# Kernel tuning notes

Hardware: AMD Instinct MI355X
Metric: run time of the kernel (lower is better)

The kernel has to match this reference:

```python
import jax, jax.numpy as jnp
import numpy as np

TRAIN_WAY = 5
TRAIN_SHOT = 5
N_LOCAL = 100  # == h*w, so Conv1d(kernel=stride=n_local) pools each class segment


def setup_inputs() -> dict:
    key = jax.random.key(0)
    k1, k2, k3 = jax.random.split(key, 3)
    t, wq, ws, c, h, w = 4, 75, 25, 640, 10, 10
    return {
        "query_feat": jax.random.normal(k1, (t, wq, c, h, w), dtype=jnp.float32),
        "support_feat": jax.random.normal(k2, (t, ws, c, h, w), dtype=jnp.float32),
        "conv_w": jax.random.normal(k3, (1, 1, N_LOCAL), dtype=jnp.float32) * 0.1,
        "conv_b": jnp.zeros((1,), dtype=jnp.float32),
    }


def reference(query_feat, support_feat, conv_w, conv_b):
    t, wq, c, h, w = query_feat.shape
    hw = h * w
    way, shot = TRAIN_WAY, TRAIN_SHOT

    # ---- support covariance per (t, way) ----
    s = support_feat.reshape(t, way * shot, c, hw).transpose(0, 1, 3, 2)  # (t, ws, hw, c)
    s = s.reshape(t, way, shot * hw, c)
    s = s - jnp.mean(s, axis=2, keepdims=True)
    cov = jnp.einsum('twnc,twnd->twcd', s, s) / (hw - 1)  # (t, way, c, c)

    # ---- query features centered over spatial positions ----
    q = query_feat.reshape(t, wq, c, hw).transpose(0, 1, 3, 2)  # (t, wq, hw, c)
    q = q - jnp.mean(q, axis=2, keepdims=True)

    # diag(Q @ Cov @ Q^T) == sum((Q @ Cov) * Q, -1)  -- same math, no hw x hw intermediate
    qc = jnp.einsum('tqnc,twcd->tqwnd', q, cov)          # (t, wq, way, hw, c)
    cov_sim = jnp.sum(qc * q[:, :, None], axis=-1)       # (t, wq, way, hw)

    # ---- LeakyReLU(0.2) -> Dropout (eval: identity) -> Conv1d(k=stride=hw) ----
    x = jnp.where(cov_sim >= 0, cov_sim, 0.2 * cov_sim)
    # conv with kernel=stride=hw over length way*hw == per-segment dot product
    score = jnp.einsum('tqwn,n->tqw', x, conv_w[0, 0]) + conv_b[0]
    return score  # (t, wq, way)
```

## Files before the change

kernel.cpp:

```cpp
#include <hip/hip_runtime.h>

#define T     4
#define WQ    75
#define C     640
#define HW    100
#define WAY   5
#define SHOT  5
#define NT    5
#define NPAIR 15

#define QOCT  14
#define QTS   (QOCT*128*8)
#define SOCT  64
#define STS   (SOCT*128*8)

#define WS_COVB_OFF  0
#define WS_QTB_OFF   9830400
#define WS_QTBW_OFF  52838400
#define WS_STB_OFF   95846400

typedef __attribute__((ext_vector_type(8)))  short bfrag8;
typedef __attribute__((ext_vector_type(16))) float f32x16;

__device__ __forceinline__ unsigned short f2bf(float x) {
    unsigned int u = __float_as_uint(x);
    return (unsigned short)((u + 0x7fffu + ((u >> 16) & 1u)) >> 16);
}
__device__ __forceinline__ float bflo(unsigned u) { return __uint_as_float(u << 16); }
__device__ __forceinline__ float bfhi(unsigned u) { return __uint_as_float(u & 0xffff0000u); }

__device__ __forceinline__ void pair_ij(int p, int& ti, int& tj) {
    int base = 0;
    #pragma unroll
    for (int a = 0; a < NT; ++a) {
        int cnt = NT - a;
        if (p < base + cnt) { ti = a; tj = a + (p - base); return; }
        base += cnt;
    }
    ti = 0; tj = 0;
}

#define LD2S 505
#define SROWS 8
#define NSPACK (20 * (C / SROWS))
struct SpackSh { float ld2[SROWS * LD2S]; float mpart2[SROWS][32]; float mean2[SROWS]; };
struct QpackSh { float ld[32 * 101]; float wl[HW]; float mpart[32][4]; float mean[32]; };
union PackSh { SpackSh s; QpackSh q; };

__global__ __launch_bounds__(256, 8)
void pack_kernel(const float* __restrict__ qf, const float* __restrict__ sf,
                 const float* __restrict__ convw, const float* __restrict__ bias,
                 unsigned short* __restrict__ stb, unsigned short* __restrict__ qtb,
                 unsigned short* __restrict__ qtbw, float* __restrict__ out) {
    __shared__ PackSh sh;
    int bid = blockIdx.x, tid = threadIdx.x;

    if (bid < NSPACK) {
        int rb = bid % 80, tw = bid / 80;
        int r0 = rb * SROWS;
        for (int sh_i = 0; sh_i < SHOT; ++sh_i) {
            const float* src = sf + ((size_t)(tw * SHOT + sh_i) * C + r0) * HW;
            if (tid < 200) {
                float4 v = ((const float4*)src)[tid];
                int f = tid * 4;
                int row = f / HW, n = f % HW;
                float* d = &sh.s.ld2[row * LD2S + sh_i * HW + n];
                d[0] = v.x; d[1] = v.y; d[2] = v.z; d[3] = v.w;
            }
        }
        __syncthreads();
        {
            int row = tid & 7, part = tid >> 3;
            float ps = 0.f;
            #pragma unroll
            for (int i = 0; i < 16; ++i) {
                int k = part * 16 + i;
                if (k < 500) ps += sh.s.ld2[row * LD2S + k];
            }
            sh.s.mpart2[row][part] = ps;
        }
        __syncthreads();
        if (tid < SROWS) {
            float s2 = 0.f;
            #pragma unroll
            for (int p2 = 0; p2 < 32; ++p2) s2 += sh.s.mpart2[tid][p2];
            sh.s.mean2[tid] = s2 * (1.0f / (SHOT * HW));
        }
        __syncthreads();
        #pragma unroll
        for (int it = 0; it < 2; ++it) {
            int task = tid + it * 256;
            int row = task & 7, oct = task >> 3;
            float m = sh.s.mean2[row];
            unsigned short ob[8] __attribute__((aligned(16)));
            #pragma unroll
            for (int j = 0; j < 8; ++j) {
                int k = oct * 8 + j;
                ob[j] = (k < 500) ? f2bf(sh.s.ld2[row * LD2S + k] - m) : (unsigned short)0;
            }
            int crow = r0 + row;
            int tile = crow >> 7, trow = crow & 127;
            size_t dst = ((((size_t)tw * NT + tile) * SOCT + oct) * 128 + trow) * 8;
            *(uint4*)(stb + dst) = *(uint4*)ob;
        }
    } else {
        int idx0 = bid - NSPACK;
        int cb = idx0 % 20, tq = idx0 / 20;
        if (idx0 == 0) {
            float b = bias[0];
            for (int i = tid; i < T * WQ * WAY; i += 256) out[i] = b;
        }
        if (tid < HW) sh.q.wl[tid] = convw[tid];
        const float* src = qf + ((size_t)tq * C + cb * 32) * HW;
        #pragma unroll
        for (int it = 0; it < 4; ++it) {
            int idx = tid + it * 256;
            if (idx < 800) {
                float4 v = ((const float4*)src)[idx];
                int f = idx * 4;
                int row = f / HW, n = f % HW;
                float* d = &sh.q.ld[row * 101 + n];
                d[0] = v.x; d[1] = v.y; d[2] = v.z; d[3] = v.w;
            }
        }
        __syncthreads();
        if (tid < 128) {
            int row = tid & 31, part = tid >> 5;
            float ps = 0.f;
            #pragma unroll
            for (int i = 0; i < 25; ++i) ps += sh.q.ld[row * 101 + part * 25 + i];
            sh.q.mpart[row][part] = ps;
        }
        __syncthreads();
        if (tid < 32) sh.q.mean[tid] = (sh.q.mpart[tid][0] + sh.q.mpart[tid][1]
                                      + sh.q.mpart[tid][2] + sh.q.mpart[tid][3]) * (1.0f / HW);
        __syncthreads();
        int crow0 = cb * 32;
        int tile = crow0 >> 7, trowbase = crow0 & 127;
        #pragma unroll
        for (int it = 0; it < 2; ++it) {
            int task = tid + it * 256;
            if (task < 32 * QOCT) {
                int row = task & 31, oct = task >> 5;
                float m = sh.q.mean[row];
                unsigned short ob[8] __attribute__((aligned(16)));
                unsigned short ow[8] __attribute__((aligned(16)));
                #pragma unroll
                for (int j = 0; j < 8; ++j) {
                    int n = oct * 8 + j;
                    float v = (n < HW) ? (sh.q.ld[row * 101 + n] - m) : 0.f;
                    float w = (n < HW) ? sh.q.wl[n] : 0.f;
                    ob[j] = f2bf(v); ow[j] = f2bf(v * w);
                }
                size_t dst = ((((size_t)tq * NT + tile) * QOCT + oct) * 128 + trowbase + row) * 8;
                *(uint4*)(qtb + dst)  = *(uint4*)ob;
                *(uint4*)(qtbw + dst) = *(uint4*)ow;
            }
        }
    }
}

__global__ __launch_bounds__(256, 3)
void cov_kernel(const unsigned short* __restrict__ stb, unsigned short* __restrict__ covb) {
    int bid = blockIdx.x, tid = threadIdx.x;
    int p = bid % NPAIR, tw = bid / NPAIR;
    int ti, tj; pair_ij(p, ti, tj);
    int lane = tid & 63, wave = tid >> 6;
    int qm = wave & 1, qn = wave >> 1, lh = lane >> 5, ls = lane & 31;
    int rA = qm * 64 + ls, rB = qn * 64 + ls;
    const unsigned short* Ab = stb + ((size_t)tw * NT + ti) * STS;
    const unsigned short* Bb = stb + ((size_t)tw * NT + tj) * STS;

    f32x16 acc[4];
    #pragma unroll
    for (int b = 0; b < 4; ++b)
        #pragma unroll
        for (int e = 0; e < 16; ++e) acc[b][e] = 0.f;

    #pragma unroll 4
    for (int s = 0; s < 32; ++s) {
        int oc = s * 2 + lh;
        const unsigned short* ap = Ab + (size_t)oc * 1024;
        const unsigned short* bp = Bb + (size_t)oc * 1024;
        bfrag8 a0 = *(const bfrag8*)&ap[rA * 8];
        bfrag8 a1 = *(const bfrag8*)&ap[(rA + 32) * 8];
        bfrag8 b0 = *(const bfrag8*)&bp[rB * 8];
        bfrag8 b1 = *(const bfrag8*)&bp[(rB + 32) * 8];
        acc[0] = __builtin_amdgcn_mfma_f32_32x32x16_bf16(a0, b0, acc[0], 0, 0, 0);
        acc[1] = __builtin_amdgcn_mfma_f32_32x32x16_bf16(a0, b1, acc[1], 0, 0, 0);
        acc[2] = __builtin_amdgcn_mfma_f32_32x32x16_bf16(a1, b0, acc[2], 0, 0, 0);
        acc[3] = __builtin_amdgcn_mfma_f32_32x32x16_bf16(a1, b1, acc[3], 0, 0, 0);
    }

    const float inv = 1.0f / (HW - 1);
    unsigned short* cbp = covb + ((size_t)tw * NPAIR + p) * 16384;
    #pragma unroll
    for (int b = 0; b < 4; ++b) {
        unsigned ow[8];
        #pragma unroll
        for (int wd = 0; wd < 8; ++wd)
            ow[wd] = (unsigned)f2bf(acc[b][2 * wd] * inv)
                   | ((unsigned)f2bf(acc[b][2 * wd + 1] * inv) << 16);
        size_t off = (size_t)((wave * 4 + b) * 64 + lane) * 16;
        *(uint4*)(cbp + off)     = *(uint4*)&ow[0];
        *(uint4*)(cbp + off + 8) = *(uint4*)&ow[4];
    }
}

#define CSTEP (NPAIR * 16384)
#define LOADW(dst, src) { \
    _Pragma("unroll") \
    for (int b = 0; b < 4; ++b) { \
        dst[2*b]   = *(const uint4*)((src) + b * 1024); \
        dst[2*b+1] = *(const uint4*)((src) + b * 1024 + 8); } }
#define FROB(buf, sout) { \
    float s0 = 0.f, s1 = 0.f, s2 = 0.f, s3 = 0.f; \
    _Pragma("unroll") \
    for (int b = 0; b < 4; ++b) { \
        _Pragma("unroll") \
        for (int h = 0; h < 2; ++h) { \
            uint4 u = buf[2*b + h]; \
            int e = h * 8; \
            s0 += bflo(u.x) * acc[b][e + 0] + bfhi(u.x) * acc[b][e + 1]; \
            s1 += bflo(u.y) * acc[b][e + 2] + bfhi(u.y) * acc[b][e + 3]; \
            s2 += bflo(u.z) * acc[b][e + 4] + bfhi(u.z) * acc[b][e + 5]; \
            s3 += bflo(u.w) * acc[b][e + 6] + bfhi(u.w) * acc[b][e + 7]; } } \
    sout = (s0 + s1) + (s2 + s3); }

__global__ __launch_bounds__(256, 2)
void score_kernel(const unsigned short* __restrict__ qtb, const unsigned short* __restrict__ qtbw,
                  const unsigned short* __restrict__ covb, float* __restrict__ out) {
    __shared__ float red[4][WAY];
    int orig = blockIdx.x;
    int xcd = orig & 7, slot = orig >> 3;
    int wgid = (xcd < 4) ? (xcd * 563 + slot) : (2252 + (xcd - 4) * 562 + slot);
    int p = wgid % NPAIR;
    int tq = wgid / NPAIR;
    int t = tq / WQ, q = tq % WQ;
    int ti, tj; pair_ij(p, ti, tj);
    int tid = threadIdx.x, lane = tid & 63, wave = tid >> 6;
    int qm = wave & 1, qn = wave >> 1, lh = lane >> 5, ls = lane & 31;
    int rA = qm * 64 + ls, rB = qn * 64 + ls;
    float mult = (ti == tj) ? 1.0f : 2.0f;

    const unsigned short* Ab = qtbw + ((size_t)(t * WQ + q) * NT + ti) * QTS;
    const unsigned short* Bb = qtb  + ((size_t)(t * WQ + q) * NT + tj) * QTS;
    const unsigned short* cb0 = covb + ((size_t)(t * WAY) * NPAIR + p) * 16384
                              + (size_t)(wave * 4096 + lane * 16);

    uint4 cuA[8], cuB[8];
    LOADW(cuA, cb0)

    f32x16 acc[4];
    #pragma unroll
    for (int b = 0; b < 4; ++b)
        #pragma unroll
        for (int e = 0; e < 16; ++e) acc[b][e] = 0.f;

    #pragma unroll
    for (int s = 0; s < 7; ++s) {
        int oc = s * 2 + lh;
        const unsigned short* ap = Ab + (size_t)oc * 1024;
        const unsigned short* bp = Bb + (size_t)oc * 1024;
        bfrag8 a0 = *(const bfrag8*)&ap[rA * 8];
        bfrag8 a1 = *(const bfrag8*)&ap[(rA + 32) * 8];
        bfrag8 b0 = *(const bfrag8*)&bp[rB * 8];
        bfrag8 b1 = *(const bfrag8*)&bp[(rB + 32) * 8];
        acc[0] = __builtin_amdgcn_mfma_f32_32x32x16_bf16(a0, b0, acc[0], 0, 0, 0);
        acc[1] = __builtin_amdgcn_mfma_f32_32x32x16_bf16(a0, b1, acc[1], 0, 0, 0);
        acc[2] = __builtin_amdgcn_mfma_f32_32x32x16_bf16(a1, b0, acc[2], 0, 0, 0);
        acc[3] = __builtin_amdgcn_mfma_f32_32x32x16_bf16(a1, b1, acc[3], 0, 0, 0);
    }

    float sw[WAY];
    LOADW(cuB, cb0 + 1 * CSTEP)
    FROB(cuA, sw[0])
    LOADW(cuA, cb0 + 2 * CSTEP)
    FROB(cuB, sw[1])
    LOADW(cuB, cb0 + 3 * CSTEP)
    FROB(cuA, sw[2])
    LOADW(cuA, cb0 + 4 * CSTEP)
    FROB(cuB, sw[3])
    FROB(cuA, sw[4])

    #pragma unroll
    for (int w = 0; w < WAY; ++w) {
        float v = sw[w] * mult;
        #pragma unroll
        for (int off2 = 32; off2 > 0; off2 >>= 1) v += __shfl_down(v, off2);
        if (lane == 0) red[wave][w] = v;
    }
    __syncthreads();
    if (tid < WAY) {
        float tot = red[0][tid] + red[1][tid] + red[2][tid] + red[3][tid];
        atomicAdd(&out[(size_t)(t * WQ + q) * WAY + tid], tot);
    }
}

extern "C" void kernel_launch(void* const* d_in, const int* in_sizes, int n_in,
                              void* d_out, int out_size, void* d_ws, size_t ws_size,
                              hipStream_t stream) {
    const float* qf = (const float*)d_in[0];
    const float* sf = (const float*)d_in[1];
    const float* cw = (const float*)d_in[2];
    const float* cb = (const float*)d_in[3];
    float* out = (float*)d_out;

    unsigned short* covb = (unsigned short*)((char*)d_ws + WS_COVB_OFF);
    unsigned short* qtb  = (unsigned short*)((char*)d_ws + WS_QTB_OFF);
    unsigned short* qtbw = (unsigned short*)((char*)d_ws + WS_QTBW_OFF);
    unsigned short* stb  = (unsigned short*)((char*)d_ws + WS_STB_OFF);

    pack_kernel<<<NSPACK + 6000, 256, 0, stream>>>(qf, sf, cw, cb, stb, qtb, qtbw, out);
    cov_kernel<<<300, 256, 0, stream>>>(stb, covb);
    score_kernel<<<4500, 256, 0, stream>>>(qtb, qtbw, covb, out);
}
```

Baseline: 220.5 us.

## Process two queries per score block to reuse covariance tile loads

Each score_kernel block now computes the Gram tiles for two queries, q0 and q1, against the same covariance pair tile. Every covariance chunk loaded from global memory is therefore applied to both accumulators, roughly halving covariance traffic and the block count. The shared-memory reduction and barrier are replaced by per-wave atomicAdds. The cost is twice the accumulator registers (two f32x16[4] sets) under launch_bounds(256,2), which risks spills or lower occupancy. There is also a redundant duplicate computation for the padded final query.

```diff
diff --git a/kernel.cpp b/kernel.cpp
--- a/kernel.cpp
+++ b/kernel.cpp
@@ -213,87 +213,104 @@
     for (int b = 0; b < 4; ++b) { \
         dst[2*b]   = *(const uint4*)((src) + b * 1024); \
         dst[2*b+1] = *(const uint4*)((src) + b * 1024 + 8); } }
-#define FROB(buf, sout) { \
-    float s0 = 0.f, s1 = 0.f, s2 = 0.f, s3 = 0.f; \
+#define FROB2(buf, out0, out1) { \
+    float a0 = 0.f, a1 = 0.f, b0 = 0.f, b1 = 0.f; \
     _Pragma("unroll") \
     for (int b = 0; b < 4; ++b) { \
         _Pragma("unroll") \
         for (int h = 0; h < 2; ++h) { \
             uint4 u = buf[2*b + h]; \
             int e = h * 8; \
-            s0 += bflo(u.x) * acc[b][e + 0] + bfhi(u.x) * acc[b][e + 1]; \
-            s1 += bflo(u.y) * acc[b][e + 2] + bfhi(u.y) * acc[b][e + 3]; \
-            s2 += bflo(u.z) * acc[b][e + 4] + bfhi(u.z) * acc[b][e + 5]; \
-            s3 += bflo(u.w) * acc[b][e + 6] + bfhi(u.w) * acc[b][e + 7]; } } \
-    sout = (s0 + s1) + (s2 + s3); }
-
+            float xl, xh; \
+            xl = bflo(u.x); xh = bfhi(u.x); \
+            a0 += xl * acc0[b][e + 0] + xh * acc0[b][e + 1]; \
+            b0 += xl * acc1[b][e + 0] + xh * acc1[b][e + 1]; \
+            xl = bflo(u.y); xh = bfhi(u.y); \
+            a1 += xl * acc0[b][e + 2] + xh * acc0[b][e + 3]; \
+            b1 += xl * acc1[b][e + 2] + xh * acc1[b][e + 3]; \
+            xl = bflo(u.z); xh = bfhi(u.z); \
+            a0 += xl * acc0[b][e + 4] + xh * acc0[b][e + 5]; \
+            b0 += xl * acc1[b][e + 4] + xh * acc1[b][e + 5]; \
+            xl = bflo(u.w); xh = bfhi(u.w); \
+            a1 += xl * acc0[b][e + 6] + xh * acc0[b][e + 7]; \
+            b1 += xl * acc1[b][e + 6] + xh * acc1[b][e + 7]; } } \
+    out0 = a0 + a1; out1 = b0 + b1; }
+#define MFMALOOP(accv, Abp, Bbp) { \
+    _Pragma("unroll") \
+    for (int s = 0; s < 7; ++s) { \
+        int oc = s * 2 + lh; \
+        const unsigned short* ap = (Abp) + (size_t)oc * 1024; \
+        const unsigned short* bp = (Bbp) + (size_t)oc * 1024; \
+        bfrag8 fa0 = *(const bfrag8*)&ap[rA * 8]; \
+        bfrag8 fa1 = *(const bfrag8*)&ap[(rA + 32) * 8]; \
+        bfrag8 fb0 = *(const bfrag8*)&bp[rB * 8]; \
+        bfrag8 fb1 = *(const bfrag8*)&bp[(rB + 32) * 8]; \
+        accv[0] = __builtin_amdgcn_mfma_f32_32x32x16_bf16(fa0, fb0, accv[0], 0, 0, 0); \
+        accv[1] = __builtin_amdgcn_mfma_f32_32x32x16_bf16(fa0, fb1, accv[1], 0, 0, 0); \
+        accv[2] = __builtin_amdgcn_mfma_f32_32x32x16_bf16(fa1, fb0, accv[2], 0, 0, 0); \
+        accv[3] = __builtin_amdgcn_mfma_f32_32x32x16_bf16(fa1, fb1, accv[3], 0, 0, 0); } }
+
+#define NQG2 38
 __global__ __launch_bounds__(256, 2)
 void score_kernel(const unsigned short* __restrict__ qtb, const unsigned short* __restrict__ qtbw,
                   const unsigned short* __restrict__ covb, float* __restrict__ out) {
-    __shared__ float red[4][WAY];
     int orig = blockIdx.x;
     int xcd = orig & 7, slot = orig >> 3;
-    int wgid = (xcd < 4) ? (xcd * 563 + slot) : (2252 + (xcd - 4) * 562 + slot);
+    int wgid = xcd * 285 + slot;
     int p = wgid % NPAIR;
-    int tq = wgid / NPAIR;
-    int t = tq / WQ, q = tq % WQ;
+    int rest = wgid / NPAIR;
+    int qg = rest % NQG2, t = rest / NQG2;
+    int q0 = qg * 2, q1 = qg * 2 + 1;
+    int q1c = (q1 < WQ) ? q1 : q0;
     int ti, tj; pair_ij(p, ti, tj);
     int tid = threadIdx.x, lane = tid & 63, wave = tid >> 6;
     int qm = wave & 1, qn = wave >> 1, lh = lane >> 5, ls = lane & 31;
     int rA = qm * 64 + ls, rB = qn * 64 + ls;
     float mult = (ti == tj) ? 1.0f : 2.0f;
 
-    const unsigned short* Ab = qtbw + ((size_t)(t * WQ + q) * NT + ti) * QTS;
-    const unsigned short* Bb = qtb  + ((size_t)(t * WQ + q) * NT + tj) * QTS;
+    const unsigned short* Ab0 = qtbw + ((size_t)(t * WQ + q0) * NT + ti) * QTS;
+    const unsigned short* Bb0 = qtb  + ((size_t)(t * WQ + q0) * NT + tj) * QTS;
+    const unsigned short* Ab1 = qtbw + ((size_t)(t * WQ + q1c) * NT + ti) * QTS;
+    const unsigned short* Bb1 = qtb  + ((size_t)(t * WQ + q1c) * NT + tj) * QTS;
     const unsigned short* cb0 = covb + ((size_t)(t * WAY) * NPAIR + p) * 16384
                               + (size_t)(wave * 4096 + lane * 16);
 
     uint4 cuA[8], cuB[8];
     LOADW(cuA, cb0)
 
-    f32x16 acc[4];
+    f32x16 acc0[4], acc1[4];
     #pragma unroll
     for (int b = 0; b < 4; ++b)
         #pragma unroll
-        for (int e = 0; e < 16; ++e) acc[b][e] = 0.f;
-
-    #pragma unroll
-    for (int s = 0; s < 7; ++s) {
-        int oc = s * 2 + lh;
-        const unsigned short* ap = Ab + (size_t)oc * 1024;
-        const unsigned short* bp = Bb + (size_t)oc * 1024;
-        bfrag8 a0 = *(const bfrag8*)&ap[rA * 8];
-        bfrag8 a1 = *(const bfrag8*)&ap[(rA + 32) * 8];
-        bfrag8 b0 = *(const bfrag8*)&bp[rB * 8];
-        bfrag8 b1 = *(const bfrag8*)&bp[(rB + 32) * 8];
-        acc[0] = __builtin_amdgcn_mfma_f32_32x32x16_bf16(a0, b0, acc[0], 0, 0, 0);
-        acc[1] = __builtin_amdgcn_mfma_f32_32x32x16_bf16(a0, b1, acc[1], 0, 0, 0);
-        acc[2] = __builtin_amdgcn_mfma_f32_32x32x16_bf16(a1, b0, acc[2], 0, 0, 0);
-        acc[3] = __builtin_amdgcn_mfma_f32_32x32x16_bf16(a1, b1, acc[3], 0, 0, 0);
-    }
-
-    float sw[WAY];
+        for (int e = 0; e < 16; ++e) { acc0[b][e] = 0.f; acc1[b][e] = 0.f; }
+
+    MFMALOOP(acc0, Ab0, Bb0)
+    MFMALOOP(acc1, Ab1, Bb1)
+
+    float sw0[WAY], sw1[WAY];
     LOADW(cuB, cb0 + 1 * CSTEP)
-    FROB(cuA, sw[0])
+    FROB2(cuA, sw0[0], sw1[0])
     LOADW(cuA, cb0 + 2 * CSTEP)
-    FROB(cuB, sw[1])
+    FROB2(cuB, sw0[1], sw1[1])
     LOADW(cuB, cb0 + 3 * CSTEP)
-    FROB(cuA, sw[2])
+    FROB2(cuA, sw0[2], sw1[2])
     LOADW(cuA, cb0 + 4 * CSTEP)
-    FROB(cuB, sw[3])
-    FROB(cuA, sw[4])
+    FROB2(cuB, sw0[3], sw1[3])
+    FROB2(cuA, sw0[4], sw1[4])
 
     #pragma unroll
     for (int w = 0; w < WAY; ++w) {
-        float v = sw[w] * mult;
-        #pragma unroll
-        for (int off2 = 32; off2 > 0; off2 >>= 1) v += __shfl_down(v, off2);
-        if (lane == 0) red[wave][w] = v;
-    }
-    __syncthreads();
-    if (tid < WAY) {
-        float tot = red[0][tid] + red[1][tid] + red[2][tid] + red[3][tid];
-        atomicAdd(&out[(size_t)(t * WQ + q) * WAY + tid], tot);
+        float v0 = sw0[w] * mult;
+        float v1 = sw1[w] * mult;
+        #pragma unroll
+        for (int off2 = 32; off2 > 0; off2 >>= 1) {
+            v0 += __shfl_down(v0, off2);
+            v1 += __shfl_down(v1, off2);
+        }
+        if (lane == 0) {
+            atomicAdd(&out[(size_t)(t * WQ + q0) * WAY + w], v0);
+            if (q1 < WQ) atomicAdd(&out[(size_t)(t * WQ + q1) * WAY + w], v1);
+        }
     }
 }
 
@@ -313,5 +330,5 @@
 
     pack_kernel<<<NSPACK + 6000, 256, 0, stream>>>(qf, sf, cw, cb, stb, qtb, qtbw, out);
     cov_kernel<<<300, 256, 0, stream>>>(stb, covb);
-    score_kernel<<<4500, 256, 0, stream>>>(qtb, qtbw, covb, out);
-}
+    score_kernel<<<T * NQG2 * NPAIR, 256, 0, stream>>>(qtb, qtbw, covb, out);
+}
```

Measured after the change: 273.0 us. 1.24x slower.
